# Kernel tuning notes

Measured on AMD Instinct MI355X. Metric: run time of the kernel, lower is better.

Reference implementation:

```python
import jax, jax.numpy as jnp
import numpy as np

B, M, D = 4096, 200, 100          # batch, max_neighbor, embed_dim
NSYM, NENT = 100001, 5000         # num_symbols+1, num_entities


def setup_inputs() -> dict:
    key = jax.random.key(0)
    ks = jax.random.split(key, 12)
    s = 0.05  # weight init scale to keep activations sane
    return {
        "connections": jax.random.randint(ks[0], (B, M, 3), 0, NENT),
        "target": jax.random.randint(ks[1], (B, 1, 2), 0, NENT),
        "symbol_emb": jax.random.normal(ks[2], (NSYM, D), jnp.float32),
        "co_entities": jax.random.uniform(ks[3], (NENT, NENT), dtype=jnp.float32),
        "gcn_w_weight": jax.random.normal(ks[4], (D, 2 * D), jnp.float32) * s,
        "gcn_w_bias": jax.random.normal(ks[5], (D,), jnp.float32) * s,
        "gcn_b": jnp.zeros((D,), jnp.float32),
        "attn_w_weight": jax.random.normal(ks[6], (1, D), jnp.float32) * s,
        "attn_w_bias": jnp.zeros((1,), jnp.float32),
        "gate_w_weight": jax.random.normal(ks[7], (1, D), jnp.float32) * s,
        "gate_w_bias": jnp.zeros((1,), jnp.float32),
        "gate_b": jnp.zeros((1,), jnp.float32),
    }


def reference(connections, target, symbol_emb, co_entities,
              gcn_w_weight, gcn_w_bias, gcn_b,
              attn_w_weight, attn_w_bias,
              gate_w_weight, gate_w_bias, gate_b):
    # --- neighbor gather ---
    relations = connections[:, :, 1]            # [B, M]
    entities = connections[:, :, 2]             # [B, M]
    entself = connections[:, 0, 0]              # [B]
    rel_embeds = symbol_emb[relations]          # [B, M, D]
    ent_embeds = symbol_emb[entities]           # [B, M, D]
    entself_embeds = symbol_emb[entself]        # [B, D]

    # co-occurrence weights: co[b, m] = co_entities[entities[b,m], target_ent[b]]
    target_ent = target[:, 0, 0]                # [B]
    co_weight = co_entities[entities, target_ent[:, None]]  # [B, M]

    # --- linear + leaky_relu (gcn) ---
    concat = jnp.concatenate([rel_embeds, ent_embeds], axis=-1)   # [B, M, 2D]
    out = jnp.einsum('bmk,dk->bmd', concat, gcn_w_weight) + gcn_w_bias + gcn_b
    out = jax.nn.leaky_relu(out, negative_slope=0.01)             # [B, M, D]

    # --- attention over neighbors ---
    attn_out = jnp.einsum('bmd,od->bmo', out, attn_w_weight) + attn_w_bias  # [B, M, 1]
    attn_weight = jax.nn.softmax(attn_out, axis=1)
    out_attn = jnp.einsum('bmd,bmo->bd', out, attn_weight)        # [B, D]

    # --- sigmoid gate ---
    gate = jax.nn.sigmoid(out_attn @ gate_w_weight.T + gate_w_bias + gate_b)  # [B, 1]
    out_neigh = out_attn * gate

    # --- co-weighted neighbor aggregation ---
    neighbor_emb = jnp.einsum('bm,bmd->bd', co_weight, ent_embeds)  # [B, D]

    return out_neigh + entself_embeds * (1.0 - gate) + neighbor_emb
```

## Files before the change

kernel.cpp:

```cpp
#include <hip/hip_runtime.h>

#define BB   4096
#define MM   200
#define DD   100
#define NENT 5000
#define CH   50
#define NCH  4
#define LPW  27
#define PTW  101

typedef _Float16 f16x2 __attribute__((ext_vector_type(2)));
typedef unsigned uint2v __attribute__((ext_vector_type(2)));

#if defined(__has_builtin)
#if __has_builtin(__builtin_amdgcn_fdot2)
#define HAS_FDOT2 1
#endif
#endif

__device__ __forceinline__ f16x2 uh(unsigned u) { return __builtin_bit_cast(f16x2, u); }
__device__ __forceinline__ float2 h2f(f16x2 h) { return make_float2((float)h.x, (float)h.y); }


__global__ __launch_bounds__(256) void precompute_kernel(
    const float* __restrict__ sym, const float* __restrict__ W,
    const float* __restrict__ wb, const float* __restrict__ gb,
    _Float16* __restrict__ Pr, _Float16* __restrict__ PES)
{
    __shared__ _Float16 Wt[200 * 102];
    const int tid = threadIdx.x;
    for (int j = tid; j < 20000; j += 256) {
        int d = j / 200, k = j % 200;
        Wt[k * 102 + d] = (_Float16)W[j];
    }
    __syncthreads();

    const int i = blockIdx.x * 256 + tid;
    if (i >= NENT * 50) return;
    const int e = i / 50, dp = i % 50;
    const float* se = sym + e * DD;

    float pr0 = 0.f, pr1 = 0.f, pe0 = 0.f, pe1 = 0.f;
    for (int k = 0; k < 100; k++) {
        float a = se[k];
        f16x2 w01 = *(const f16x2*)&Wt[k * 102 + 2 * dp];
        f16x2 w23 = *(const f16x2*)&Wt[(k + 100) * 102 + 2 * dp];
        pr0 = fmaf(a, (float)w01.x, pr0);
        pr1 = fmaf(a, (float)w01.y, pr1);
        pe0 = fmaf(a, (float)w23.x, pe0);
        pe1 = fmaf(a, (float)w23.y, pe1);
    }
    const int d0 = 2 * dp;
    pr0 += wb[d0]     + gb[d0];
    pr1 += wb[d0 + 1] + gb[d0 + 1];

    *(f16x2*)&Pr[e * DD + d0]           = f16x2{(_Float16)pr0, (_Float16)pr1};
    *(f16x2*)&PES[e * 2 * DD + d0]      = f16x2{(_Float16)pe0, (_Float16)pe1};
    *(f16x2*)&PES[e * 2 * DD + DD + d0] = f16x2{(_Float16)se[d0], (_Float16)se[d0 + 1]};
}

__global__ __launch_bounds__(256, 6) void main_kernel(
    const int*  __restrict__ conn, const int* __restrict__ target,
    const float* __restrict__ sym, const float* __restrict__ co,
    const _Float16* __restrict__ Pr, const _Float16* __restrict__ PES,
    const float* __restrict__ attn_w,
    const float* __restrict__ gate_w, const float* __restrict__ gate_wb,
    const float* __restrict__ gate_b,
    float* __restrict__ outp)
{
    __shared__ float    scratch[2 * 10 * PTW];
    __shared__ unsigned idx_s[MM];
    __shared__ float    co_s[MM];
    __shared__ float    l_s[CH];
    __shared__ float    red[4];
    float* lp_s = scratch;
    float* part = scratch;

    const int t = threadIdx.x;
    const int b = blockIdx.x;
    const int* cb = conn + b * (MM * 3);
    const int lane = t & 63, wid = t >> 6;

    if (t < MM) {
        int r = cb[t * 3 + 1];
        int e = cb[t * 3 + 2];
        idx_s[t] = (unsigned)r | ((unsigned)e << 16);
        int tgt = target[b * 2];
        co_s[t] = co[(long)e * NENT + tgt];
    }
    __syncthreads();

    const int g = t / 25, dq = t % 25;
    const bool act = (t < 250);

    float4 awf = *(const float4*)&attn_w[4 * dq];
#ifdef HAS_FDOT2
    f16x2 aw01 = f16x2{(_Float16)awf.x, (_Float16)awf.y};
    f16x2 aw23 = f16x2{(_Float16)awf.z, (_Float16)awf.w};
#endif
    const _Float16 slope = (_Float16)0.01f;

    float oa0 = 0.f, oa1 = 0.f, oa2 = 0.f, oa3 = 0.f;
    f16x2 nb01 = f16x2{(_Float16)0.f, (_Float16)0.f};
    f16x2 nb23 = nb01;
    float run_max = -3.0e38f, run_sum = 0.f;
    uint2v xs[5];

    for (int c = 0; c < NCH; ++c) {
        if (act) {
            #pragma unroll
            for (int it = 0; it < 5; ++it) {
                int ml = g + 10 * it;
                int m = c * CH + ml;
                unsigned ir = idx_s[m];
                int r = ir & 0xffff, e = ir >> 16;
                uint2v pru = *(const uint2v*)(Pr + r * DD + 4 * dq);
                uint2v peu = *(const uint2v*)(PES + e * 2 * DD + 4 * dq);
                uint2v syu = *(const uint2v*)(PES + e * 2 * DD + DD + 4 * dq);
                f16x2 x01 = uh(pru.x) + uh(peu.x);
                f16x2 x23 = uh(pru.y) + uh(peu.y);
                x01 = __builtin_elementwise_max(x01, x01 * slope);
                x23 = __builtin_elementwise_max(x23, x23 * slope);
                xs[it].x = __builtin_bit_cast(unsigned, x01);
                xs[it].y = __builtin_bit_cast(unsigned, x23);
                float lp;
#ifdef HAS_FDOT2
                lp = __builtin_amdgcn_fdot2(x01, aw01, 0.0f, false);
                lp = __builtin_amdgcn_fdot2(x23, aw23, lp, false);
#else
                float2 f01 = h2f(x01), f23 = h2f(x23);
                lp = f01.x * awf.x + f01.y * awf.y + f23.x * awf.z + f23.y * awf.w;
#endif
                lp_s[ml * LPW + dq] = lp;
                _Float16 coh = (_Float16)co_s[m];
                f16x2 co2 = f16x2{coh, coh};
                nb01 = co2 * uh(syu.x) + nb01;
                nb23 = co2 * uh(syu.y) + nb23;
            }
        }
        __syncthreads();

        if (t < 4 * CH) {
            int ml = t >> 2, q = t & 3;
            const float* row = &lp_s[ml * LPW + ((q == 0) ? 0 : 7 + 6 * (q - 1))];
            float s = row[0] + row[1] + row[2] + row[3] + row[4] + row[5];
            if (q == 0) s += row[6];
            s += __shfl_xor(s, 1);
            s += __shfl_xor(s, 2);
            if (q == 0) l_s[ml] = s;
        }
        __syncthreads();

        float lv = (lane < CH) ? l_s[lane] : -3.0e38f;
        float mx = lv;
        for (int off = 32; off >= 1; off >>= 1) mx = fmaxf(mx, __shfl_xor(mx, off));
        float new_max = fmaxf(run_max, mx);
        float scale = __expf(run_max - new_max);
        float ev = (lane < CH) ? __expf(lv - new_max) : 0.f;
        float cs = ev;
        for (int off = 32; off >= 1; off >>= 1) cs += __shfl_xor(cs, off);
        run_sum = run_sum * scale + cs;
        run_max = new_max;
        oa0 *= scale; oa1 *= scale; oa2 *= scale; oa3 *= scale;

        if (act) {
            #pragma unroll
            for (int it = 0; it < 5; ++it) {
                int ml = g + 10 * it;
                float w = __shfl(ev, ml);
                float2 f01 = h2f(uh(xs[it].x));
                float2 f23 = h2f(uh(xs[it].y));
                oa0 = fmaf(w, f01.x, oa0);
                oa1 = fmaf(w, f01.y, oa1);
                oa2 = fmaf(w, f23.x, oa2);
                oa3 = fmaf(w, f23.y, oa3);
            }
        }
    }

    if (act) {
        float* po = &part[g * PTW + 4 * dq];
        po[0] = oa0; po[1] = oa1; po[2] = oa2; po[3] = oa3;
        float2 n01 = h2f(nb01), n23 = h2f(nb23);
        float* pn = &part[(10 + g) * PTW + 4 * dq];
        pn[0] = n01.x; pn[1] = n01.y; pn[2] = n23.x; pn[3] = n23.y;
    }
    __syncthreads();

    float inv = 1.f / run_sum;
    float oaf = 0.f, nbf = 0.f;
    if (t < DD) {
        #pragma unroll
        for (int g2 = 0; g2 < 10; ++g2) {
            oaf += part[g2 * PTW + t];
            nbf += part[(10 + g2) * PTW + t];
        }
        oaf *= inv;
    }

    float p = (t < DD) ? oaf * gate_w[t] : 0.f;
    for (int off = 32; off >= 1; off >>= 1) p += __shfl_xor(p, off);
    if (lane == 0) red[wid] = p;
    __syncthreads();
    float dot = (red[0] + red[1]) + (red[2] + red[3]);
    float gt = 1.f / (1.f + __expf(-(dot + gate_wb[0] + gate_b[0])));

    if (t < DD) {
        float self_v = sym[cb[0] * DD + t];
        outp[b * DD + t] = oaf * gt + self_v * (1.f - gt) + nbf;
    }
}

extern "C" void kernel_launch(void* const* d_in, const int* in_sizes, int n_in,
                              void* d_out, int out_size, void* d_ws, size_t ws_size,
                              hipStream_t stream) {
    const int*   conn    = (const int*)  d_in[0];
    const int*   target  = (const int*)  d_in[1];
    const float* sym     = (const float*)d_in[2];
    const float* co      = (const float*)d_in[3];
    const float* W       = (const float*)d_in[4];
    const float* wb      = (const float*)d_in[5];
    const float* gb      = (const float*)d_in[6];
    const float* attn_w  = (const float*)d_in[7];
    const float* gate_w  = (const float*)d_in[9];
    const float* gate_wb = (const float*)d_in[10];
    const float* gate_b  = (const float*)d_in[11];

    _Float16* Pr  = (_Float16*)d_ws;
    _Float16* PES = (_Float16*)((char*)d_ws + 1000000);

    precompute_kernel<<<(NENT * 50 + 255) / 256, 256, 0, stream>>>(
        sym, W, wb, gb, Pr, PES);

    main_kernel<<<BB, 256, 0, stream>>>(
        conn, target, sym, co, Pr, PES,
        attn_w, gate_w, gate_wb, gate_b, (float*)d_out);
}
```

Baseline: 70.31 us.

## Replace chunked online softmax with single-pass full-neighbor softmax

Removes the 4-chunk online-softmax loop and its per-chunk barriers and rescaling. Each thread now gathers and keeps all 20 of its neighbor activations in registers. The 200 logits are then reduced in one pass, and a block-wide max and sum are taken via wave shuffles plus shared memory. Cuts barrier count and puts more independent gathers in flight, at the cost of higher register pressure and larger LDS use. The launch-bounds occupancy hint drops from 6 to 4 blocks.

```diff
diff --git a/kernel.cpp b/kernel.cpp
--- a/kernel.cpp
+++ b/kernel.cpp
@@ -4,8 +4,6 @@
 #define MM   200
 #define DD   100
 #define NENT 5000
-#define CH   50
-#define NCH  4
 #define LPW  27
 #define PTW  101
 
@@ -59,7 +57,7 @@
     *(f16x2*)&PES[e * 2 * DD + DD + d0] = f16x2{(_Float16)se[d0], (_Float16)se[d0 + 1]};
 }
 
-__global__ __launch_bounds__(256, 6) void main_kernel(
+__global__ __launch_bounds__(256, 4) void main_kernel(
     const int*  __restrict__ conn, const int* __restrict__ target,
     const float* __restrict__ sym, const float* __restrict__ co,
     const _Float16* __restrict__ Pr, const _Float16* __restrict__ PES,
@@ -68,11 +66,11 @@
     const float* __restrict__ gate_b,
     float* __restrict__ outp)
 {
-    __shared__ float    scratch[2 * 10 * PTW];
+    __shared__ float    scratch[MM * LPW];
     __shared__ unsigned idx_s[MM];
     __shared__ float    co_s[MM];
-    __shared__ float    l_s[CH];
-    __shared__ float    red[4];
+    __shared__ float    ev_s[MM];
+    __shared__ float    red[8];
     float* lp_s = scratch;
     float* part = scratch;
 
@@ -100,83 +98,83 @@
 #endif
     const _Float16 slope = (_Float16)0.01f;
 
-    float oa0 = 0.f, oa1 = 0.f, oa2 = 0.f, oa3 = 0.f;
     f16x2 nb01 = f16x2{(_Float16)0.f, (_Float16)0.f};
     f16x2 nb23 = nb01;
-    float run_max = -3.0e38f, run_sum = 0.f;
-    uint2v xs[5];
-
-    for (int c = 0; c < NCH; ++c) {
-        if (act) {
-            #pragma unroll
-            for (int it = 0; it < 5; ++it) {
-                int ml = g + 10 * it;
-                int m = c * CH + ml;
-                unsigned ir = idx_s[m];
-                int r = ir & 0xffff, e = ir >> 16;
-                uint2v pru = *(const uint2v*)(Pr + r * DD + 4 * dq);
-                uint2v peu = *(const uint2v*)(PES + e * 2 * DD + 4 * dq);
-                uint2v syu = *(const uint2v*)(PES + e * 2 * DD + DD + 4 * dq);
-                f16x2 x01 = uh(pru.x) + uh(peu.x);
-                f16x2 x23 = uh(pru.y) + uh(peu.y);
-                x01 = __builtin_elementwise_max(x01, x01 * slope);
-                x23 = __builtin_elementwise_max(x23, x23 * slope);
-                xs[it].x = __builtin_bit_cast(unsigned, x01);
-                xs[it].y = __builtin_bit_cast(unsigned, x23);
-                float lp;
+    uint2v xs[20];
+
+    if (act) {
+        #pragma unroll
+        for (int it = 0; it < 20; ++it) {
+            int m = g + 10 * it;
+            unsigned ir = idx_s[m];
+            int r = ir & 0xffff, e = ir >> 16;
+            uint2v pru = *(const uint2v*)(Pr + r * DD + 4 * dq);
+            uint2v peu = *(const uint2v*)(PES + e * 2 * DD + 4 * dq);
+            uint2v syu = *(const uint2v*)(PES + e * 2 * DD + DD + 4 * dq);
+            f16x2 x01 = uh(pru.x) + uh(peu.x);
+            f16x2 x23 = uh(pru.y) + uh(peu.y);
+            x01 = __builtin_elementwise_max(x01, x01 * slope);
+            x23 = __builtin_elementwise_max(x23, x23 * slope);
+            xs[it].x = __builtin_bit_cast(unsigned, x01);
+            xs[it].y = __builtin_bit_cast(unsigned, x23);
+            float lp;
 #ifdef HAS_FDOT2
-                lp = __builtin_amdgcn_fdot2(x01, aw01, 0.0f, false);
-                lp = __builtin_amdgcn_fdot2(x23, aw23, lp, false);
+            lp = __builtin_amdgcn_fdot2(x01, aw01, 0.0f, false);
+            lp = __builtin_amdgcn_fdot2(x23, aw23, lp, false);
 #else
-                float2 f01 = h2f(x01), f23 = h2f(x23);
-                lp = f01.x * awf.x + f01.y * awf.y + f23.x * awf.z + f23.y * awf.w;
-#endif
-                lp_s[ml * LPW + dq] = lp;
-                _Float16 coh = (_Float16)co_s[m];
-                f16x2 co2 = f16x2{coh, coh};
-                nb01 = co2 * uh(syu.x) + nb01;
-                nb23 = co2 * uh(syu.y) + nb23;
-            }
+            float2 f01 = h2f(x01), f23 = h2f(x23);
+            lp = f01.x * awf.x + f01.y * awf.y + f23.x * awf.z + f23.y * awf.w;
+#endif
+            lp_s[m * LPW + dq] = lp;
+            _Float16 coh = (_Float16)co_s[m];
+            f16x2 co2 = f16x2{coh, coh};
+            nb01 = co2 * uh(syu.x) + nb01;
+            nb23 = co2 * uh(syu.y) + nb23;
         }
-        __syncthreads();
-
-        if (t < 4 * CH) {
-            int ml = t >> 2, q = t & 3;
-            const float* row = &lp_s[ml * LPW + ((q == 0) ? 0 : 7 + 6 * (q - 1))];
-            float s = row[0] + row[1] + row[2] + row[3] + row[4] + row[5];
-            if (q == 0) s += row[6];
-            s += __shfl_xor(s, 1);
-            s += __shfl_xor(s, 2);
-            if (q == 0) l_s[ml] = s;
+    }
+    __syncthreads();
+
+    float logit = -3.0e38f;
+    if (t < MM) {
+        const float* row = &lp_s[t * LPW];
+        float s0 = (row[0] + row[1]) + (row[2] + row[3]);
+        float s1 = (row[4] + row[5]) + (row[6] + row[7]);
+        float s2 = (row[8] + row[9]) + (row[10] + row[11]);
+        float s3 = (row[12] + row[13]) + (row[14] + row[15]);
+        float s4 = (row[16] + row[17]) + (row[18] + row[19]);
+        float s5 = (row[20] + row[21]) + (row[22] + row[23]);
+        logit = ((s0 + s1) + (s2 + s3)) + ((s4 + s5) + row[24]);
+    }
+
+    float v = logit;
+    for (int off = 32; off >= 1; off >>= 1) v = fmaxf(v, __shfl_xor(v, off));
+    if (lane == 0) red[wid] = v;
+    __syncthreads();
+    float gmax = fmaxf(fmaxf(red[0], red[1]), fmaxf(red[2], red[3]));
+    float ev = (t < MM) ? __expf(logit - gmax) : 0.f;
+    if (t < MM) ev_s[t] = ev;
+    float s = ev;
+    for (int off = 32; off >= 1; off >>= 1) s += __shfl_xor(s, off);
+    if (lane == 0) red[4 + wid] = s;
+    __syncthreads();
+    float gsum = (red[4] + red[5]) + (red[6] + red[7]);
+
+    float oa0 = 0.f, oa1 = 0.f, oa2 = 0.f, oa3 = 0.f;
+    if (act) {
+        #pragma unroll
+        for (int it = 0; it < 20; ++it) {
+            int m = g + 10 * it;
+            float w = ev_s[m];
+            float2 f01 = h2f(uh(xs[it].x));
+            float2 f23 = h2f(uh(xs[it].y));
+            oa0 = fmaf(w, f01.x, oa0);
+            oa1 = fmaf(w, f01.y, oa1);
+            oa2 = fmaf(w, f23.x, oa2);
+            oa3 = fmaf(w, f23.y, oa3);
         }
-        __syncthreads();
-
-        float lv = (lane < CH) ? l_s[lane] : -3.0e38f;
-        float mx = lv;
-        for (int off = 32; off >= 1; off >>= 1) mx = fmaxf(mx, __shfl_xor(mx, off));
-        float new_max = fmaxf(run_max, mx);
-        float scale = __expf(run_max - new_max);
-        float ev = (lane < CH) ? __expf(lv - new_max) : 0.f;
-        float cs = ev;
-        for (int off = 32; off >= 1; off >>= 1) cs += __shfl_xor(cs, off);
-        run_sum = run_sum * scale + cs;
-        run_max = new_max;
-        oa0 *= scale; oa1 *= scale; oa2 *= scale; oa3 *= scale;
-
-        if (act) {
-            #pragma unroll
-            for (int it = 0; it < 5; ++it) {
-                int ml = g + 10 * it;
-                float w = __shfl(ev, ml);
-                float2 f01 = h2f(uh(xs[it].x));
-                float2 f23 = h2f(uh(xs[it].y));
-                oa0 = fmaf(w, f01.x, oa0);
-                oa1 = fmaf(w, f01.y, oa1);
-                oa2 = fmaf(w, f23.x, oa2);
-                oa3 = fmaf(w, f23.y, oa3);
-            }
-        }
-    }
+    }
+    float inv = 1.f / gsum;
+    oa0 *= inv; oa1 *= inv; oa2 *= inv; oa3 *= inv;
 
     if (act) {
         float* po = &part[g * PTW + 4 * dq];
@@ -187,7 +185,6 @@
     }
     __syncthreads();
 
-    float inv = 1.f / run_sum;
     float oaf = 0.f, nbf = 0.f;
     if (t < DD) {
         #pragma unroll
@@ -195,7 +192,6 @@
             oaf += part[g2 * PTW + t];
             nbf += part[(10 + g2) * PTW + t];
         }
-        oaf *= inv;
     }
 
     float p = (t < DD) ? oaf * gate_w[t] : 0.f;
```

New measurement: 65.91 us. 1.07x faster.
